# Kernel optimization log

Hardware: AMD Instinct MI355X
Metric: run time of the kernel (lower is better)

## Reference

```python
import jax, jax.numpy as jnp
import numpy as np

EPS = 1e-3
MAX_ITER = 100
STAB = 1e-8


def setup_inputs() -> dict:
    key = jax.random.key(0)
    k1, k2 = jax.random.split(key)
    x = jax.random.normal(k1, (4, 4096, 8, 8), dtype=jnp.float32)
    y = jax.random.normal(k2, (4, 4096, 8, 8), dtype=jnp.float32)
    return {"x": x, "y": y}


def _sinkhorn_distance(x, y):
    B, N, H, W = x.shape
    d = H * W
    xf = jax.nn.softmax(x.reshape(B, N, d), axis=-1)  # [B,N,d]
    yf = jax.nn.softmax(y.reshape(B, N, d), axis=-1)  # [B,N,d]

    # squared euclidean distance: ||a-b||^2 = ||a||^2 + ||b||^2 - 2 a.b  (== cdist(p=2)**2)
    x2 = jnp.sum(xf * xf, axis=-1)  # [B,N]
    y2 = jnp.sum(yf * yf, axis=-1)  # [B,N]
    cross = jnp.einsum('bid,bjd->bij', xf, yf)  # [B,N,N]
    cost = jnp.maximum(x2[:, :, None] + y2[:, None, :] - 2.0 * cross, 0.0)

    K = jnp.exp(-cost / EPS)  # [B,N,N]

    u0 = jnp.full((B, N), 1.0 / N, dtype=x.dtype)
    v0 = jnp.full((B, N), 1.0 / N, dtype=x.dtype)

    def step(carry, _):
        u, v = carry
        u = 1.0 / (jnp.einsum('bij,bj->bi', K, v) + STAB)
        v = 1.0 / (jnp.einsum('bij,bi->bj', K, u) + STAB)
        return (u, v), None

    (u, v), _ = jax.lax.scan(step, (u0, v0), None, length=MAX_ITER)

    plan = u[:, :, None] * K * v[:, None, :]  # [B,N,N]
    dist = jnp.sum(plan * cost, axis=(1, 2))  # [B]
    return jnp.sum(dist)  # reduction='sum'


def reference(x, y):
    return _sinkhorn_distance(x, y)
```

## Files before the change

kernel.cpp:

```cpp
#include <hip/hip_runtime.h>
#include <stdint.h>

#define BB 4
#define NN 4096
#define DD 64
#define BN (BB*NN)
#define STABF 1e-8f
#define NITER 100
#define NEG_SCALE (-1442.695040888963f)

__device__ __forceinline__ float bf16lo(uint32_t w){ return __uint_as_float(w << 16); }
__device__ __forceinline__ float bf16hi(uint32_t w){ return __uint_as_float(w & 0xffff0000u); }
__device__ __forceinline__ uint32_t pack2bf(float f0, float f1){
  uint32_t u0 = __float_as_uint(f0); u0 += 0x7fffu + ((u0 >> 16) & 1u);
  uint32_t u1 = __float_as_uint(f1); u1 += 0x7fffu + ((u1 >> 16) & 1u);
  return (u0 >> 16) | (u1 & 0xffff0000u);
}

__global__ __launch_bounds__(256) void k_init(float* __restrict__ acc0,
                                              float* __restrict__ partial) {
  int idx = blockIdx.x * 256 + threadIdx.x;
  if (idx < BN) acc0[idx] = (float)NN;
  if (idx < 256) partial[idx] = 0.f;
}

__global__ __launch_bounds__(256) void k_softmax(
    const float* __restrict__ x, const float* __restrict__ y,
    float* __restrict__ xf, float* __restrict__ yf,
    float* __restrict__ x2, float* __restrict__ y2) {
  int wave = (blockIdx.x * 256 + threadIdx.x) >> 6;
  int lane = threadIdx.x & 63;
  const float* src; float* dst; float* d2; int row;
  if (wave < BN) { src = x; dst = xf; d2 = x2; row = wave; }
  else           { src = y; dst = yf; d2 = y2; row = wave - BN; }
  float v = src[(size_t)row * DD + lane];
  float m = v;
  #pragma unroll
  for (int off = 32; off; off >>= 1) m = fmaxf(m, __shfl_xor(m, off));
  float e = __expf(v - m);
  float s = e;
  #pragma unroll
  for (int off = 32; off; off >>= 1) s += __shfl_xor(s, off);
  float p = e / s;
  dst[(size_t)row * DD + lane] = p;
  float q = p * p;
  #pragma unroll
  for (int off = 32; off; off >>= 1) q += __shfl_xor(q, off);
  if (lane == 0) d2[row] = q;
}

__device__ __forceinline__ void fma_row(float av0, float av1, const float4 bv,
                                        float cr0[4], float cr1[4]) {
  cr0[0] = fmaf(av0, bv.x, cr0[0]); cr0[1] = fmaf(av0, bv.y, cr0[1]);
  cr0[2] = fmaf(av0, bv.z, cr0[2]); cr0[3] = fmaf(av0, bv.w, cr0[3]);
  cr1[0] = fmaf(av1, bv.x, cr1[0]); cr1[1] = fmaf(av1, bv.y, cr1[1]);
  cr1[2] = fmaf(av1, bv.z, cr1[2]); cr1[3] = fmaf(av1, bv.w, cr1[3]);
}

__global__ __launch_bounds__(256) void k_build(
    const float* __restrict__ xf, const float* __restrict__ yf,
    const float* __restrict__ x2, const float* __restrict__ y2,
    unsigned short* __restrict__ K) {
  __shared__ float sxf[32][68];
  __shared__ float syt[64][68];
  int bid = blockIdx.x, t = threadIdx.x;
  int jt = bid & 63, it = (bid >> 6) & 127, b = bid >> 13;
  int i0 = it * 32, j0 = jt * 64;
  {
    int r = t >> 3, c = (t & 7) * 8;
    const float* s0 = xf + ((size_t)(b*NN + i0 + r)) * DD + c;
    *(float4*)&sxf[r][c]     = *(const float4*)s0;
    *(float4*)&sxf[r][c + 4] = *(const float4*)(s0 + 4);
  }
  {
    int r = t >> 2, c0 = (t & 3) * 16;
    const float* s0 = yf + ((size_t)(b*NN + j0 + r)) * DD + c0;
    #pragma unroll
    for (int q = 0; q < 4; ++q) {
      float4 pv = *(const float4*)(s0 + q*4);
      syt[c0 + q*4 + 0][r] = pv.x;
      syt[c0 + q*4 + 1][r] = pv.y;
      syt[c0 + q*4 + 2][r] = pv.z;
      syt[c0 + q*4 + 3][r] = pv.w;
    }
  }
  __syncthreads();
  int tx = t & 15, ty = t >> 4;
  int ii = ty * 2, jj = tx * 4;
  float cr[2][4] = {{0,0,0,0},{0,0,0,0}};
  #pragma unroll
  for (int d = 0; d < DD; d += 4) {
    float4 a0 = *(const float4*)&sxf[ii][d];
    float4 a1 = *(const float4*)&sxf[ii + 1][d];
    float4 b0 = *(const float4*)&syt[d][jj];
    float4 b1 = *(const float4*)&syt[d + 1][jj];
    float4 b2 = *(const float4*)&syt[d + 2][jj];
    float4 b3 = *(const float4*)&syt[d + 3][jj];
    fma_row(a0.x, a1.x, b0, cr[0], cr[1]);
    fma_row(a0.y, a1.y, b1, cr[0], cr[1]);
    fma_row(a0.z, a1.z, b2, cr[0], cr[1]);
    fma_row(a0.w, a1.w, b3, cr[0], cr[1]);
  }
  float x2v[2], y2v[4];
  x2v[0] = x2[b*NN + i0 + ii]; x2v[1] = x2[b*NN + i0 + ii + 1];
  #pragma unroll
  for (int c = 0; c < 4; ++c) y2v[c] = y2[b*NN + j0 + jj + c];
  #pragma unroll
  for (int i2 = 0; i2 < 2; ++i2) {
    float k4[4];
    #pragma unroll
    for (int c = 0; c < 4; ++c) {
      float cost = fmaxf(x2v[i2] + y2v[c] - 2.f * cr[i2][c], 0.f);
      k4[c] = exp2f(cost * NEG_SCALE);
    }
    uint2 kw;
    kw.x = pack2bf(k4[0], k4[1]);
    kw.y = pack2bf(k4[2], k4[3]);
    *(uint2*)(K + ((size_t)(b*NN + i0 + ii + i2)) * NN + j0 + jj) = kw;
  }
}

__global__ __launch_bounds__(256) void k_rowdot(
    const unsigned short* __restrict__ K, const float* __restrict__ accIn,
    float* __restrict__ u, float* __restrict__ accZ) {
  int bid = blockIdx.x, t = threadIdx.x;
  if (bid < 16) {
    float4 z = make_float4(0.f, 0.f, 0.f, 0.f);
    *(float4*)(accZ + (size_t)(bid * 256 + t) * 4) = z;
  }
  int row = bid * 4 + (t >> 6);
  int lane = t & 63;
  const unsigned short* Kp = K + (size_t)row * NN;
  const float* ap = accIn + (size_t)(row >> 12) * NN;
  float sum = 0.f;
  #pragma unroll
  for (int itn = 0; itn < 8; ++itn) {
    int j = itn * 512 + lane * 8;
    uint4 kw = *(const uint4*)(Kp + j);
    float4 av0 = *(const float4*)(ap + j);
    float4 av1 = *(const float4*)(ap + j + 4);
    float v0 = __builtin_amdgcn_rcpf(av0.x + STABF);
    float v1 = __builtin_amdgcn_rcpf(av0.y + STABF);
    float v2 = __builtin_amdgcn_rcpf(av0.z + STABF);
    float v3 = __builtin_amdgcn_rcpf(av0.w + STABF);
    float v4 = __builtin_amdgcn_rcpf(av1.x + STABF);
    float v5 = __builtin_amdgcn_rcpf(av1.y + STABF);
    float v6 = __builtin_amdgcn_rcpf(av1.z + STABF);
    float v7 = __builtin_amdgcn_rcpf(av1.w + STABF);
    sum = fmaf(bf16lo(kw.x), v0, sum);
    sum = fmaf(bf16hi(kw.x), v1, sum);
    sum = fmaf(bf16lo(kw.y), v2, sum);
    sum = fmaf(bf16hi(kw.y), v3, sum);
    sum = fmaf(bf16lo(kw.z), v4, sum);
    sum = fmaf(bf16hi(kw.z), v5, sum);
    sum = fmaf(bf16lo(kw.w), v6, sum);
    sum = fmaf(bf16hi(kw.w), v7, sum);
  }
  #pragma unroll
  for (int off = 32; off; off >>= 1) sum += __shfl_xor(sum, off);
  if (lane == 0) u[row] = 1.0f / (sum + STABF);
}

__global__ __launch_bounds__(256) void k_coldot(
    const unsigned short* __restrict__ K, const float* __restrict__ u,
    float* __restrict__ acc) {
  int bid = blockIdx.x, t = threadIdx.x;
  int slab = bid & 1, chunk = (bid >> 1) & 63, b = bid >> 7;
  int i0 = chunk * 64;
  int j0 = slab * 2048 + t * 8;
  const unsigned short* Kp = K + ((size_t)(b*NN + i0)) * NN + j0;
  const float* up = u + b*NN + i0;
  float s0=0,s1=0,s2=0,s3=0,s4=0,s5=0,s6=0,s7=0;
  #pragma unroll 4
  for (int r = 0; r < 64; ++r) {
    uint4 kw = *(const uint4*)(Kp + (size_t)r * NN);
    float ur = up[r];
    s0 = fmaf(bf16lo(kw.x), ur, s0);
    s1 = fmaf(bf16hi(kw.x), ur, s1);
    s2 = fmaf(bf16lo(kw.y), ur, s2);
    s3 = fmaf(bf16hi(kw.y), ur, s3);
    s4 = fmaf(bf16lo(kw.z), ur, s4);
    s5 = fmaf(bf16hi(kw.z), ur, s5);
    s6 = fmaf(bf16lo(kw.w), ur, s6);
    s7 = fmaf(bf16hi(kw.w), ur, s7);
  }
  float* ap = acc + b*NN + j0;
  atomicAdd(ap + 0, s0); atomicAdd(ap + 1, s1);
  atomicAdd(ap + 2, s2); atomicAdd(ap + 3, s3);
  atomicAdd(ap + 4, s4); atomicAdd(ap + 5, s5);
  atomicAdd(ap + 6, s6); atomicAdd(ap + 7, s7);
}

__global__ __launch_bounds__(256) void k_final(
    const float* __restrict__ xf, const float* __restrict__ yf,
    const float* __restrict__ x2, const float* __restrict__ y2,
    const unsigned short* __restrict__ K, const float* __restrict__ u,
    const float* __restrict__ accv, float* __restrict__ partial) {
  __shared__ float sxf[32][68];
  __shared__ float syt[64][68];
  __shared__ float red[256];
  int bid = blockIdx.x, t = threadIdx.x;
  int jt = bid & 63, it = (bid >> 6) & 127, b = bid >> 13;
  int i0 = it * 32, j0 = jt * 64;
  {
    int r = t >> 3, c = (t & 7) * 8;
    const float* s0 = xf + ((size_t)(b*NN + i0 + r)) * DD + c;
    *(float4*)&sxf[r][c]     = *(const float4*)s0;
    *(float4*)&sxf[r][c + 4] = *(const float4*)(s0 + 4);
  }
  {
    int r = t >> 2, c0 = (t & 3) * 16;
    const float* s0 = yf + ((size_t)(b*NN + j0 + r)) * DD + c0;
    #pragma unroll
    for (int q = 0; q < 4; ++q) {
      float4 pv = *(const float4*)(s0 + q*4);
      syt[c0 + q*4 + 0][r] = pv.x;
      syt[c0 + q*4 + 1][r] = pv.y;
      syt[c0 + q*4 + 2][r] = pv.z;
      syt[c0 + q*4 + 3][r] = pv.w;
    }
  }
  __syncthreads();
  int tx = t & 15, ty = t >> 4;
  int ii = ty * 2, jj = tx * 4;
  float cr[2][4] = {{0,0,0,0},{0,0,0,0}};
  #pragma unroll
  for (int d = 0; d < DD; d += 4) {
    float4 a0 = *(const float4*)&sxf[ii][d];
    float4 a1 = *(const float4*)&sxf[ii + 1][d];
    float4 b0 = *(const float4*)&syt[d][jj];
    float4 b1 = *(const float4*)&syt[d + 1][jj];
    float4 b2 = *(const float4*)&syt[d + 2][jj];
    float4 b3 = *(const float4*)&syt[d + 3][jj];
    fma_row(a0.x, a1.x, b0, cr[0], cr[1]);
    fma_row(a0.y, a1.y, b1, cr[0], cr[1]);
    fma_row(a0.z, a1.z, b2, cr[0], cr[1]);
    fma_row(a0.w, a1.w, b3, cr[0], cr[1]);
  }
  float x2v[2], y2v[4], uv[2], vv[4];
  x2v[0] = x2[b*NN + i0 + ii]; x2v[1] = x2[b*NN + i0 + ii + 1];
  uv[0]  = u[b*NN + i0 + ii];  uv[1]  = u[b*NN + i0 + ii + 1];
  #pragma unroll
  for (int c = 0; c < 4; ++c) {
    y2v[c] = y2[b*NN + j0 + jj + c];
    vv[c]  = __builtin_amdgcn_rcpf(accv[b*NN + j0 + jj + c] + STABF);
  }
  float s = 0.f;
  #pragma unroll
  for (int i2 = 0; i2 < 2; ++i2) {
    uint2 kw = *(const uint2*)(K + ((size_t)(b*NN + i0 + ii + i2)) * NN + j0 + jj);
    float kk[4] = {bf16lo(kw.x), bf16hi(kw.x), bf16lo(kw.y), bf16hi(kw.y)};
    #pragma unroll
    for (int c = 0; c < 4; ++c) {
      float cost = fmaxf(x2v[i2] + y2v[c] - 2.f * cr[i2][c], 0.f);
      s = fmaf(uv[i2] * kk[c] * vv[c], cost, s);
    }
  }
  red[t] = s;
  __syncthreads();
  #pragma unroll
  for (int off = 128; off; off >>= 1) {
    if (t < off) red[t] += red[t + off];
    __syncthreads();
  }
  if (t == 0) atomicAdd(partial + (bid & 255), red[0]);
}

__global__ __launch_bounds__(256) void k_finalize(const float* __restrict__ partial,
                                                 float* __restrict__ out) {
  __shared__ float red[256];
  int t = threadIdx.x;
  red[t] = partial[t];
  __syncthreads();
  #pragma unroll
  for (int off = 128; off; off >>= 1) {
    if (t < off) red[t] += red[t + off];
    __syncthreads();
  }
  if (t == 0) out[0] = red[0];
}

extern "C" void kernel_launch(void* const* d_in, const int* in_sizes, int n_in,
                              void* d_out, int out_size, void* d_ws, size_t ws_size,
                              hipStream_t stream) {
  const float* x = (const float*)d_in[0];
  const float* y = (const float*)d_in[1];
  float* out = (float*)d_out;

  char* w = (char*)d_ws;
  unsigned short* K = (unsigned short*)w;
  float* xf = (float*)(w + (size_t)BN * NN * 2);
  float* yf = xf + (size_t)BN * DD;
  float* x2 = yf + (size_t)BN * DD;
  float* y2 = x2 + BN;
  float* uu = y2 + BN;
  float* acc = uu + BN;
  float* partial = acc + 2 * BN;
  (void)in_sizes; (void)n_in; (void)out_size; (void)ws_size;

  k_init<<<64, 256, 0, stream>>>(acc, partial);
  k_softmax<<<8192, 256, 0, stream>>>(x, y, xf, yf, x2, y2);
  k_build<<<32768, 256, 0, stream>>>(xf, yf, x2, y2, K);

  int p = 0;
  for (int itr = 0; itr < NITER; ++itr) {
    k_rowdot<<<4096, 256, 0, stream>>>(K, acc + (size_t)p * BN, uu, acc + (size_t)(1 - p) * BN);
    k_coldot<<<512, 256, 0, stream>>>(K, uu, acc + (size_t)(1 - p) * BN);
    p ^= 1;
  }
  k_final<<<32768, 256, 0, stream>>>(xf, yf, x2, y2, K, uu, acc, partial);
  k_finalize<<<1, 256, 0, stream>>>(partial, out);
}
```

Before: 7.310 ms.

## Fuse row and column Sinkhorn passes into one kernel reading K once

Merges the row-dot and column-dot kernels so each block loads a strip of K rows once, computes u for each row, and reuses the same K registers to accumulate column partial sums. Column partials are reduced in shared memory with atomics and then atomically added to global accumulators rotated across three buffers. This targets halving K bandwidth per iteration at the cost of high register pressure and many atomics.

Result: faster. 6.842 ms (-6.4%).

```diff
diff --git a/kernel.cpp b/kernel.cpp
--- a/kernel.cpp
+++ b/kernel.cpp
@@ -16,11 +16,16 @@
   uint32_t u1 = __float_as_uint(f1); u1 += 0x7fffu + ((u1 >> 16) & 1u);
   return (u0 >> 16) | (u1 & 0xffff0000u);
 }
-
-__global__ __launch_bounds__(256) void k_init(float* __restrict__ acc0,
+__device__ __forceinline__ int swz(int c){ return c ^ ((c >> 5) & 7); }
+
+__global__ __launch_bounds__(256) void k_init(float* __restrict__ acc,
                                               float* __restrict__ partial) {
   int idx = blockIdx.x * 256 + threadIdx.x;
-  if (idx < BN) acc0[idx] = (float)NN;
+  if (idx < BN) {
+    acc[idx] = (float)NN;
+    acc[BN + idx] = 0.f;
+    acc[2 * BN + idx] = 0.f;
+  }
   if (idx < 256) partial[idx] = 0.f;
 }
 
@@ -120,75 +125,93 @@
   }
 }
 
-__global__ __launch_bounds__(256) void k_rowdot(
-    const unsigned short* __restrict__ K, const float* __restrict__ accIn,
-    float* __restrict__ u, float* __restrict__ accZ) {
+__global__ __launch_bounds__(256, 2) void k_iter(
+    const unsigned short* __restrict__ K,
+    const float* __restrict__ accIn,
+    float* __restrict__ accOut,
+    float* __restrict__ accZ,
+    float* __restrict__ u) {
+  __shared__ float sacc[NN];
   int bid = blockIdx.x, t = threadIdx.x;
+  int wv = t >> 6, lane = t & 63;
   if (bid < 16) {
-    float4 z = make_float4(0.f, 0.f, 0.f, 0.f);
-    *(float4*)(accZ + (size_t)(bid * 256 + t) * 4) = z;
-  }
-  int row = bid * 4 + (t >> 6);
-  int lane = t & 63;
-  const unsigned short* Kp = K + (size_t)row * NN;
-  const float* ap = accIn + (size_t)(row >> 12) * NN;
-  float sum = 0.f;
+    *(float4*)(accZ + (size_t)(bid * 256 + t) * 4) = make_float4(0.f, 0.f, 0.f, 0.f);
+  }
+  #pragma unroll
+  for (int q = 0; q < 16; ++q) sacc[q * 256 + t] = 0.f;
+
+  int b = bid >> 7;
+  int row0 = (bid & 127) * 32 + wv * 8;
+  const float* ap = accIn + (size_t)b * NN + lane * 8;
+  float vv[64];
   #pragma unroll
   for (int itn = 0; itn < 8; ++itn) {
-    int j = itn * 512 + lane * 8;
-    uint4 kw = *(const uint4*)(Kp + j);
-    float4 av0 = *(const float4*)(ap + j);
-    float4 av1 = *(const float4*)(ap + j + 4);
-    float v0 = __builtin_amdgcn_rcpf(av0.x + STABF);
-    float v1 = __builtin_amdgcn_rcpf(av0.y + STABF);
-    float v2 = __builtin_amdgcn_rcpf(av0.z + STABF);
-    float v3 = __builtin_amdgcn_rcpf(av0.w + STABF);
-    float v4 = __builtin_amdgcn_rcpf(av1.x + STABF);
-    float v5 = __builtin_amdgcn_rcpf(av1.y + STABF);
-    float v6 = __builtin_amdgcn_rcpf(av1.z + STABF);
-    float v7 = __builtin_amdgcn_rcpf(av1.w + STABF);
-    sum = fmaf(bf16lo(kw.x), v0, sum);
-    sum = fmaf(bf16hi(kw.x), v1, sum);
-    sum = fmaf(bf16lo(kw.y), v2, sum);
-    sum = fmaf(bf16hi(kw.y), v3, sum);
-    sum = fmaf(bf16lo(kw.z), v4, sum);
-    sum = fmaf(bf16hi(kw.z), v5, sum);
-    sum = fmaf(bf16lo(kw.w), v6, sum);
-    sum = fmaf(bf16hi(kw.w), v7, sum);
-  }
-  #pragma unroll
-  for (int off = 32; off; off >>= 1) sum += __shfl_xor(sum, off);
-  if (lane == 0) u[row] = 1.0f / (sum + STABF);
-}
-
-__global__ __launch_bounds__(256) void k_coldot(
-    const unsigned short* __restrict__ K, const float* __restrict__ u,
-    float* __restrict__ acc) {
-  int bid = blockIdx.x, t = threadIdx.x;
-  int slab = bid & 1, chunk = (bid >> 1) & 63, b = bid >> 7;
-  int i0 = chunk * 64;
-  int j0 = slab * 2048 + t * 8;
-  const unsigned short* Kp = K + ((size_t)(b*NN + i0)) * NN + j0;
-  const float* up = u + b*NN + i0;
-  float s0=0,s1=0,s2=0,s3=0,s4=0,s5=0,s6=0,s7=0;
-  #pragma unroll 4
-  for (int r = 0; r < 64; ++r) {
-    uint4 kw = *(const uint4*)(Kp + (size_t)r * NN);
-    float ur = up[r];
-    s0 = fmaf(bf16lo(kw.x), ur, s0);
-    s1 = fmaf(bf16hi(kw.x), ur, s1);
-    s2 = fmaf(bf16lo(kw.y), ur, s2);
-    s3 = fmaf(bf16hi(kw.y), ur, s3);
-    s4 = fmaf(bf16lo(kw.z), ur, s4);
-    s5 = fmaf(bf16hi(kw.z), ur, s5);
-    s6 = fmaf(bf16lo(kw.w), ur, s6);
-    s7 = fmaf(bf16hi(kw.w), ur, s7);
-  }
-  float* ap = acc + b*NN + j0;
-  atomicAdd(ap + 0, s0); atomicAdd(ap + 1, s1);
-  atomicAdd(ap + 2, s2); atomicAdd(ap + 3, s3);
-  atomicAdd(ap + 4, s4); atomicAdd(ap + 5, s5);
-  atomicAdd(ap + 6, s6); atomicAdd(ap + 7, s7);
+    float4 a0 = *(const float4*)(ap + itn * 512);
+    float4 a1 = *(const float4*)(ap + itn * 512 + 4);
+    vv[itn*8+0] = __builtin_amdgcn_rcpf(a0.x + STABF);
+    vv[itn*8+1] = __builtin_amdgcn_rcpf(a0.y + STABF);
+    vv[itn*8+2] = __builtin_amdgcn_rcpf(a0.z + STABF);
+    vv[itn*8+3] = __builtin_amdgcn_rcpf(a0.w + STABF);
+    vv[itn*8+4] = __builtin_amdgcn_rcpf(a1.x + STABF);
+    vv[itn*8+5] = __builtin_amdgcn_rcpf(a1.y + STABF);
+    vv[itn*8+6] = __builtin_amdgcn_rcpf(a1.z + STABF);
+    vv[itn*8+7] = __builtin_amdgcn_rcpf(a1.w + STABF);
+  }
+  float ca[64];
+  #pragma unroll
+  for (int q = 0; q < 64; ++q) ca[q] = 0.f;
+  __syncthreads();
+
+  const unsigned short* Kbase = K + (size_t)(b * NN + row0) * NN + lane * 8;
+  float* urow = u + b * NN + row0;
+  #pragma unroll 1
+  for (int r = 0; r < 8; ++r) {
+    const unsigned short* Kp = Kbase + (size_t)r * NN;
+    uint4 kw[8];
+    #pragma unroll
+    for (int itn = 0; itn < 8; ++itn) kw[itn] = *(const uint4*)(Kp + itn * 512);
+    float sum = 0.f;
+    #pragma unroll
+    for (int itn = 0; itn < 8; ++itn) {
+      sum = fmaf(bf16lo(kw[itn].x), vv[itn*8+0], sum);
+      sum = fmaf(bf16hi(kw[itn].x), vv[itn*8+1], sum);
+      sum = fmaf(bf16lo(kw[itn].y), vv[itn*8+2], sum);
+      sum = fmaf(bf16hi(kw[itn].y), vv[itn*8+3], sum);
+      sum = fmaf(bf16lo(kw[itn].z), vv[itn*8+4], sum);
+      sum = fmaf(bf16hi(kw[itn].z), vv[itn*8+5], sum);
+      sum = fmaf(bf16lo(kw[itn].w), vv[itn*8+6], sum);
+      sum = fmaf(bf16hi(kw[itn].w), vv[itn*8+7], sum);
+    }
+    #pragma unroll
+    for (int off = 32; off; off >>= 1) sum += __shfl_xor(sum, off);
+    float ur = 1.0f / (sum + STABF);
+    if (lane == 0) urow[r] = ur;
+    #pragma unroll
+    for (int itn = 0; itn < 8; ++itn) {
+      ca[itn*8+0] = fmaf(bf16lo(kw[itn].x), ur, ca[itn*8+0]);
+      ca[itn*8+1] = fmaf(bf16hi(kw[itn].x), ur, ca[itn*8+1]);
+      ca[itn*8+2] = fmaf(bf16lo(kw[itn].y), ur, ca[itn*8+2]);
+      ca[itn*8+3] = fmaf(bf16hi(kw[itn].y), ur, ca[itn*8+3]);
+      ca[itn*8+4] = fmaf(bf16lo(kw[itn].z), ur, ca[itn*8+4]);
+      ca[itn*8+5] = fmaf(bf16hi(kw[itn].z), ur, ca[itn*8+5]);
+      ca[itn*8+6] = fmaf(bf16lo(kw[itn].w), ur, ca[itn*8+6]);
+      ca[itn*8+7] = fmaf(bf16hi(kw[itn].w), ur, ca[itn*8+7]);
+    }
+  }
+  int cbase = lane * 8;
+  #pragma unroll
+  for (int itn = 0; itn < 8; ++itn) {
+    #pragma unroll
+    for (int q = 0; q < 8; ++q)
+      atomicAdd(&sacc[swz(itn * 512 + cbase + q)], ca[itn*8+q]);
+  }
+  __syncthreads();
+  float* op = accOut + (size_t)b * NN;
+  #pragma unroll
+  for (int q = 0; q < 16; ++q) {
+    int c = q * 256 + t;
+    atomicAdd(op + c, sacc[swz(c)]);
+  }
 }
 
 __global__ __launch_bounds__(256) void k_final(
@@ -295,19 +318,21 @@
   float* y2 = x2 + BN;
   float* uu = y2 + BN;
   float* acc = uu + BN;
-  float* partial = acc + 2 * BN;
+  float* partial = acc + 3 * BN;
   (void)in_sizes; (void)n_in; (void)out_size; (void)ws_size;
 
   k_init<<<64, 256, 0, stream>>>(acc, partial);
   k_softmax<<<8192, 256, 0, stream>>>(x, y, xf, yf, x2, y2);
   k_build<<<32768, 256, 0, stream>>>(xf, yf, x2, y2, K);
 
-  int p = 0;
   for (int itr = 0; itr < NITER; ++itr) {
-    k_rowdot<<<4096, 256, 0, stream>>>(K, acc + (size_t)p * BN, uu, acc + (size_t)(1 - p) * BN);
-    k_coldot<<<512, 256, 0, stream>>>(K, uu, acc + (size_t)(1 - p) * BN);
-    p ^= 1;
-  }
-  k_final<<<32768, 256, 0, stream>>>(xf, yf, x2, y2, K, uu, acc, partial);
+    int rB = itr % 3, wB = (itr + 1) % 3, zB = (itr + 2) % 3;
+    k_iter<<<512, 256, 0, stream>>>(K,
+                                    acc + (size_t)rB * BN,
+                                    acc + (size_t)wB * BN,
+                                    acc + (size_t)zB * BN,
+                                    uu);
+  }
+  k_final<<<32768, 256, 0, stream>>>(xf, yf, x2, y2, K, uu, acc + BN, partial);
   k_finalize<<<1, 256, 0, stream>>>(partial, out);
 }
```
